# Optimization experiments

Hardware: AMD Instinct MI355X
Metric: run time of the kernel (lower is better)

## Reference

```python
import jax, jax.numpy as jnp
import numpy as np

B, S, D, H = 2048, 200, 64, 4
H1, H2 = 64, 32
F = 4 * D


def _prelu(x, a):
    return jnp.where(x > 0, x, a * x)


def setup_inputs() -> dict:
    key = jax.random.key(0)
    ks = jax.random.split(key, 12)
    inp = {
        "query": jax.random.normal(ks[0], (B, D), dtype=jnp.float32),
        "keys": jax.random.normal(ks[1], (B, S, D), dtype=jnp.float32),
        "keys_mask": jax.random.randint(ks[2], (B, S), 0, 2, dtype=jnp.int32),
        # per-head MLP params (torch Linear equivalent, stored as [in,out])
        "W1": jax.random.normal(ks[3], (H, F, H1), dtype=jnp.float32) / np.sqrt(F),
        "b1": jnp.zeros((H, H1), dtype=jnp.float32),
        "a1": jnp.full((H,), 0.25, dtype=jnp.float32),  # PReLU weight
        "W2": jax.random.normal(ks[4], (H, H1, H2), dtype=jnp.float32) / np.sqrt(H1),
        "b2": jnp.zeros((H, H2), dtype=jnp.float32),
        "a2": jnp.full((H,), 0.25, dtype=jnp.float32),
        "W3": jax.random.normal(ks[5], (H, H2), dtype=jnp.float32) / np.sqrt(H2),
        "b3": jnp.zeros((H,), dtype=jnp.float32),
        # output projection
        "Wo": jax.random.normal(ks[6], (D, D), dtype=jnp.float32) / np.sqrt(D),
        "bo": jnp.zeros((D,), dtype=jnp.float32),
    }
    return inp


def reference(query, keys, keys_mask, W1, b1, a1, W2, b2, a2, W3, b3, Wo, bo):
    # rich attention features: [keys, q, keys*q, keys-q] -> [B,S,4D]
    q = jnp.broadcast_to(query[:, None, :], keys.shape)
    x = jnp.concatenate([keys, q, keys * q, keys - q], axis=-1)
    # all heads at once: tiny per-head MLP with PReLU
    h = jnp.einsum('bsf,hfk->bhsk', x, W1) + b1[None, :, None, :]   # [B,H,S,H1]
    h = _prelu(h, a1[None, :, None, None])
    h = jnp.einsum('bhsk,hkm->bhsm', h, W2) + b2[None, :, None, :]  # [B,H,S,H2]
    h = _prelu(h, a2[None, :, None, None])
    scores = jnp.einsum('bhsm,hm->bhs', h, W3) + b3[None, :, None]  # [B,H,S]
    # mask + softmax + NaN->0 (all-masked rows)
    valid = (keys_mask != 0)[:, None, :]
    scores = jnp.where(valid, scores, -jnp.inf)
    w = jax.nn.softmax(scores, axis=-1)
    w = jnp.where(jnp.isnan(w), jnp.zeros_like(w), w)
    # weighted sum over keys, mean over heads
    out_h = jnp.einsum('bhs,bsd->bhd', w, keys)  # [B,H,D]
    combined = out_h.mean(axis=1)                # [B,D]
    return combined @ Wo + bo
```

## Files before the change

kernel.cpp:

```cpp
#include <hip/hip_runtime.h>
#include <math.h>

constexpr int B  = 2048;
constexpr int S  = 200;
constexpr int D  = 64;
constexpr int H  = 4;
constexpr int H1 = 64;
constexpr int H2 = 32;
constexpr int F  = 256;

constexpr int PK = 72;

typedef short bf16x8 __attribute__((ext_vector_type(8)));
typedef float f32x4  __attribute__((ext_vector_type(4)));
typedef unsigned uint4v __attribute__((ext_vector_type(4)));

__device__ __forceinline__ unsigned cvtpk(float a, float b) {
    unsigned r;
    asm volatile("v_cvt_pk_bf16_f32 %0, %1, %2" : "=v"(r) : "v"(a), "v"(b));
    return r;
}
__device__ __forceinline__ float lo16f(unsigned w) { return __builtin_bit_cast(float, w << 16); }
__device__ __forceinline__ float hi16f(unsigned w) { return __builtin_bit_cast(float, w & 0xffff0000u); }

constexpr size_t SAD_OFF = 0;
constexpr size_t SC_OFF  = SAD_OFF + 4 * 4096 * 4;
constexpr size_t SBD_OFF = SC_OFF  + 4 * 4096 * 4;
constexpr size_t W2I_OFF = SBD_OFF + 4 * 4096 * 4;

__global__ __launch_bounds__(256) void build_kernel(
    const float* __restrict__ W1, const float* __restrict__ W2,
    float* __restrict__ sad, float* __restrict__ sc, float* __restrict__ sbd,
    ushort* __restrict__ w2i)
{
    const int h    = blockIdx.x >> 1;
    const int half = blockIdx.x & 1;
    const int t = threadIdx.x;
    const float* w1h = W1 + (size_t)h * F * H1;

    {
        const int sl = half * 256 + t;
        const int f  = sl >> 6, l = sl & 63;
        const int mt = f & 3, kk = f >> 2;
        const int k  = 16 * mt + (l & 15);
        const int d0 = 32 * kk + ((l >> 4) << 3);
        float vs[8], vc[8], vb[8];
        #pragma unroll
        for (int j = 0; j < 8; ++j) {
            const int d = d0 + j;
            float A  = w1h[d * 64 + k];
            float Bv = w1h[(64 + d) * 64 + k];
            float C  = w1h[(128 + d) * 64 + k];
            float Dv = w1h[(192 + d) * 64 + k];
            vs[j] = A + Dv; vc[j] = C; vb[j] = Bv - Dv;
        }
        const size_t off = ((size_t)h * 512 + sl) * 8;
        *(f32x4*)&sad[off]     = *(f32x4*)&vs[0];
        *(f32x4*)&sad[off + 4] = *(f32x4*)&vs[4];
        *(f32x4*)&sc [off]     = *(f32x4*)&vc[0];
        *(f32x4*)&sc [off + 4] = *(f32x4*)&vc[4];
        *(f32x4*)&sbd[off]     = *(f32x4*)&vb[0];
        *(f32x4*)&sbd[off + 4] = *(f32x4*)&vb[4];
    }

    if (half == 0) {
        const int f2 = t >> 6, l = t & 63;
        const int mt2 = f2 & 1, w = f2 >> 1;
        const int m = 16 * mt2 + (l & 15), k20 = 32 * w + ((l >> 4) << 3);
        const float* w2h = W2 + (size_t)h * H1 * H2;
        uint4v u = { cvtpk(w2h[(k20 + 0) * 32 + m], w2h[(k20 + 1) * 32 + m]),
                     cvtpk(w2h[(k20 + 2) * 32 + m], w2h[(k20 + 3) * 32 + m]),
                     cvtpk(w2h[(k20 + 4) * 32 + m], w2h[(k20 + 5) * 32 + m]),
                     cvtpk(w2h[(k20 + 6) * 32 + m], w2h[(k20 + 7) * 32 + m]) };
        *(uint4v*)&w2i[((size_t)h * 4 + f2) * 512 + l * 8] = u;
    }
}

__global__ __launch_bounds__(256, 3) void fused_b_kernel(
    const float* __restrict__ query, const float* __restrict__ keys,
    const int* __restrict__ mask,
    const float* __restrict__ sad, const float* __restrict__ sc,
    const float* __restrict__ sbd, const ushort* __restrict__ w2i,
    const float* __restrict__ b1, const float* __restrict__ a1,
    const float* __restrict__ b2, const float* __restrict__ a2,
    const float* __restrict__ W3, const float* __restrict__ b3,
    const float* __restrict__ Wo, const float* __restrict__ bo,
    float* __restrict__ out)
{
    __shared__ ushort sK[200 * PK];
    __shared__ ushort relay[4][16 * PK];

    const int b    = blockIdx.x;
    const int t    = threadIdx.x;
    const int lane = t & 63;
    const int h    = t >> 6;
    const int g    = lane >> 4;
    const int ln16 = lane & 15;

    unsigned mbits = 0;
    {
        int mval[4];
        #pragma unroll
        for (int c = 0; c < 4; ++c) {
            int s = lane + 64 * c;
            mval[c] = (s < S) ? mask[(size_t)b * S + s] : 0;
        }
        #pragma unroll
        for (int st = 0; st < 13; ++st) {
            const int src = 16 * (st & 3) + ln16;
            int v = (st >> 2) == 0 ? __shfl(mval[0], src)
                  : (st >> 2) == 1 ? __shfl(mval[1], src)
                  : (st >> 2) == 2 ? __shfl(mval[2], src)
                  :                  __shfl(mval[3], src);
            mbits |= (v != 0) ? (1u << st) : 0u;
        }
    }

    {
        const float4* k4 = (const float4*)(keys + (size_t)b * S * D);
        float4 kv[6];
        #pragma unroll
        for (int i = 0; i < 6; ++i) kv[i] = k4[t + 256 * i];
        #pragma unroll
        for (int i = 0; i < 6; ++i) {
            const int idx = t + 256 * i;
            const int s = idx >> 4, dc = (idx & 15) * 4;
            *(uint2*)&sK[s * PK + dc] =
                make_uint2(cvtpk(kv[i].x, kv[i].y), cvtpk(kv[i].z, kv[i].w));
        }
        #pragma unroll
        for (int i = 0; i < 6; ++i) kv[i] = k4[t + 256 * (6 + i)];
        #pragma unroll
        for (int i = 0; i < 6; ++i) {
            const int idx = t + 256 * (6 + i);
            const int s = idx >> 4, dc = (idx & 15) * 4;
            *(uint2*)&sK[s * PK + dc] =
                make_uint2(cvtpk(kv[i].x, kv[i].y), cvtpk(kv[i].z, kv[i].w));
        }
        if (t < 128) {
            float4 kt = k4[3072 + t];
            const int idx = 3072 + t;
            const int s = idx >> 4, dc = (idx & 15) * 4;
            *(uint2*)&sK[s * PK + dc] =
                make_uint2(cvtpk(kt.x, kt.y), cvtpk(kt.z, kt.w));
        }
    }

    const float* qb = query + (size_t)b * D;
    bf16x8 wh[4][2];
    float qtp0 = 0.f, qtp1 = 0.f, qtp2 = 0.f, qtp3 = 0.f;
    #pragma unroll
    for (int kk = 0; kk < 2; ++kk) {
        const int d0 = 32 * kk + 8 * g;
        f32x4 q0 = *(const f32x4*)&qb[d0];
        f32x4 q1 = *(const f32x4*)&qb[d0 + 4];
        #pragma unroll
        for (int mt = 0; mt < 4; ++mt) {
            const int f = kk * 4 + mt;
            const size_t off = ((size_t)h * 512 + f * 64 + lane) * 8;
            f32x4 s0 = *(const f32x4*)&sad[off], s1 = *(const f32x4*)&sad[off + 4];
            f32x4 c0 = *(const f32x4*)&sc [off], c1 = *(const f32x4*)&sc [off + 4];
            f32x4 bd0 = *(const f32x4*)&sbd[off], bd1 = *(const f32x4*)&sbd[off + 4];
            float w0 = s0[0] + q0[0] * c0[0], w1 = s0[1] + q0[1] * c0[1];
            float w2 = s0[2] + q0[2] * c0[2], w3 = s0[3] + q0[3] * c0[3];
            float w4 = s1[0] + q1[0] * c1[0], w5 = s1[1] + q1[1] * c1[1];
            float w6 = s1[2] + q1[2] * c1[2], w7 = s1[3] + q1[3] * c1[3];
            uint4v u = { cvtpk(w0, w1), cvtpk(w2, w3), cvtpk(w4, w5), cvtpk(w6, w7) };
            wh[mt][kk] = __builtin_bit_cast(bf16x8, u);
            float d = q0[0]*bd0[0] + q0[1]*bd0[1] + q0[2]*bd0[2] + q0[3]*bd0[3]
                    + q1[0]*bd1[0] + q1[1]*bd1[1] + q1[2]*bd1[2] + q1[3]*bd1[3];
            if (mt == 0) qtp0 += d; else if (mt == 1) qtp1 += d;
            else if (mt == 2) qtp2 += d; else qtp3 += d;
        }
    }
    qtp0 += __shfl_xor(qtp0, 16); qtp0 += __shfl_xor(qtp0, 32);
    qtp1 += __shfl_xor(qtp1, 16); qtp1 += __shfl_xor(qtp1, 32);
    qtp2 += __shfl_xor(qtp2, 16); qtp2 += __shfl_xor(qtp2, 32);
    qtp3 += __shfl_xor(qtp3, 16); qtp3 += __shfl_xor(qtp3, 32);
    f32x4 qtv[4];
    #pragma unroll
    for (int mt = 0; mt < 4; ++mt) {
        float src = (mt == 0) ? qtp0 : (mt == 1) ? qtp1 : (mt == 2) ? qtp2 : qtp3;
        f32x4 b1v = *(const f32x4*)&b1[h * 64 + mt * 16 + 4 * g];
        f32x4 v;
        #pragma unroll
        for (int i = 0; i < 4; ++i) v[i] = __shfl(src, 4 * g + i) + b1v[i];
        qtv[mt] = v;
    }

    bf16x8 w2f[2][2];
    #pragma unroll
    for (int w = 0; w < 2; ++w)
        #pragma unroll
        for (int mt2 = 0; mt2 < 2; ++mt2)
            w2f[w][mt2] = *(const bf16x8*)&w2i[((size_t)h * 4 + w * 2 + mt2) * 512 + lane * 8];
    f32x4 b2v[2], w3v[2];
    #pragma unroll
    for (int mt2 = 0; mt2 < 2; ++mt2) {
        b2v[mt2] = *(const f32x4*)&b2[h * 32 + mt2 * 16 + 4 * g];
        w3v[mt2] = *(const f32x4*)&W3[h * 32 + mt2 * 16 + 4 * g];
    }
    const float a1v = a1[h], a2v = a2[h], b3v = b3[h];

    __syncthreads();

    ushort* myR = relay[h];
    float sc13[13];

    #pragma unroll
    for (int st = 0; st < 13; ++st) {
        int srow = st * 16 + ln16;
        srow = srow > 199 ? 199 : srow;
        bf16x8 bk0 = *(const bf16x8*)&sK[srow * PK + 0  + 8 * g];
        bf16x8 bk1 = *(const bf16x8*)&sK[srow * PK + 32 + 8 * g];

        f32x4 acc[4] = { qtv[0], qtv[1], qtv[2], qtv[3] };
        #pragma unroll
        for (int mt = 0; mt < 4; ++mt)
            acc[mt] = __builtin_amdgcn_mfma_f32_16x16x32_bf16(wh[mt][0], bk0, acc[mt], 0, 0, 0);
        #pragma unroll
        for (int mt = 0; mt < 4; ++mt)
            acc[mt] = __builtin_amdgcn_mfma_f32_16x16x32_bf16(wh[mt][1], bk1, acc[mt], 0, 0, 0);

        #pragma unroll
        for (int mt = 0; mt < 4; ++mt) {
            float v0 = fmaxf(acc[mt][0], acc[mt][0] * a1v);
            float v1 = fmaxf(acc[mt][1], acc[mt][1] * a1v);
            float v2 = fmaxf(acc[mt][2], acc[mt][2] * a1v);
            float v3 = fmaxf(acc[mt][3], acc[mt][3] * a1v);
            *(uint2*)&myR[ln16 * PK + mt * 16 + 4 * g] =
                make_uint2(cvtpk(v0, v1), cvtpk(v2, v3));
        }

        f32x4 acc2[2] = { b2v[0], b2v[1] };
        #pragma unroll
        for (int w = 0; w < 2; ++w) {
            bf16x8 Bh = *(const bf16x8*)&myR[ln16 * PK + w * 32 + 8 * g];
            #pragma unroll
            for (int mt2 = 0; mt2 < 2; ++mt2)
                acc2[mt2] = __builtin_amdgcn_mfma_f32_16x16x32_bf16(w2f[w][mt2], Bh, acc2[mt2], 0, 0, 0);
        }

        float part = 0.f;
        #pragma unroll
        for (int mt2 = 0; mt2 < 2; ++mt2) {
            #pragma unroll
            for (int i2 = 0; i2 < 4; ++i2) {
                float v = fmaxf(acc2[mt2][i2], acc2[mt2][i2] * a2v);
                part += v * w3v[mt2][i2];
            }
        }
        part += __shfl_xor(part, 16);
        part += __shfl_xor(part, 32);
        sc13[st] = part + b3v;
    }

    float* ws = (float*)myR;
    {
        float M = -INFINITY;
        #pragma unroll
        for (int st = 0; st < 13; ++st)
            if ((mbits >> st) & 1) M = fmaxf(M, sc13[st]);
        #pragma unroll
        for (int off = 1; off < 16; off <<= 1) M = fmaxf(M, __shfl_xor(M, off));
        float Z = 0.f;
        #pragma unroll
        for (int st = 0; st < 13; ++st)
            Z += ((mbits >> st) & 1) ? __expf(sc13[st] - M) : 0.f;
        #pragma unroll
        for (int off = 1; off < 16; off <<= 1) Z += __shfl_xor(Z, off);
        const float inv = Z > 0.f ? 1.f / Z : 0.f;
        if (g == 0) {
            #pragma unroll
            for (int st = 0; st < 13; ++st) {
                const int s = st * 16 + ln16;
                if (st < 12 || ln16 < 8)
                    ws[s] = ((mbits >> st) & 1) ? __expf(sc13[st] - M) * inv : 0.f;
            }
        }
    }

    {
        const int sg = lane >> 4, dq = ln16;
        float ax = 0.f, ay = 0.f, az = 0.f, aw = 0.f;
        #pragma unroll 5
        for (int i = 0; i < 50; ++i) {
            const int s = sg * 50 + i;
            const float w = ws[s];
            uint2 kv = *(const uint2*)&sK[s * PK + 4 * dq];
            ax += w * lo16f(kv.x); ay += w * hi16f(kv.x);
            az += w * lo16f(kv.y); aw += w * hi16f(kv.y);
        }
        ax += __shfl_xor(ax, 16); ay += __shfl_xor(ay, 16);
        az += __shfl_xor(az, 16); aw += __shfl_xor(aw, 16);
        ax += __shfl_xor(ax, 32); ay += __shfl_xor(ay, 32);
        az += __shfl_xor(az, 32); aw += __shfl_xor(aw, 32);
        if (lane < 16) {
            float4 o = { ax, ay, az, aw };
            *(float4*)&ws[200 + 4 * dq] = o;
        }
    }
    __syncthreads();

    {
        float p = 0.f;
        #pragma unroll
        for (int j = 0; j < 16; ++j) {
            const int d = 16 * h + j;
            const float cmb = 0.25f * (((const float*)relay[0])[200 + d]
                                     + ((const float*)relay[1])[200 + d]
                                     + ((const float*)relay[2])[200 + d]
                                     + ((const float*)relay[3])[200 + d]);
            p += cmb * Wo[d * 64 + lane];
        }
        ws[264 + lane] = p;
    }
    __syncthreads();
    if (t < 64) {
        float o = bo[t] + ((const float*)relay[0])[264 + t]
                        + ((const float*)relay[1])[264 + t]
                        + ((const float*)relay[2])[264 + t]
                        + ((const float*)relay[3])[264 + t];
        out[(size_t)b * D + t] = o;
    }
}

extern "C" void kernel_launch(void* const* d_in, const int* in_sizes, int n_in,
                              void* d_out, int out_size, void* d_ws, size_t ws_size,
                              hipStream_t stream) {
    const float* query = (const float*)d_in[0];
    const float* keys  = (const float*)d_in[1];
    const int*   mask  = (const int*)d_in[2];
    const float* W1 = (const float*)d_in[3];
    const float* b1 = (const float*)d_in[4];
    const float* a1 = (const float*)d_in[5];
    const float* W2 = (const float*)d_in[6];
    const float* b2 = (const float*)d_in[7];
    const float* a2 = (const float*)d_in[8];
    const float* W3 = (const float*)d_in[9];
    const float* b3 = (const float*)d_in[10];
    const float* Wo = (const float*)d_in[11];
    const float* bo = (const float*)d_in[12];

    float* out  = (float*)d_out;
    char*  ws   = (char*)d_ws;
    float* sad  = (float*)(ws + SAD_OFF);
    float* sc   = (float*)(ws + SC_OFF);
    float* sbd  = (float*)(ws + SBD_OFF);
    ushort* w2i = (ushort*)(ws + W2I_OFF);

    build_kernel<<<dim3(H * 2), 256, 0, stream>>>(W1, W2, sad, sc, sbd, w2i);
    fused_b_kernel<<<dim3(B), 256, 0, stream>>>(
        query, keys, mask, sad, sc, sbd, w2i, b1, a1, b2, a2, W3, b3,
        Wo, bo, out);
}
```

Baseline: 62.08 us.

## Permute W2 rows to enable 128-bit relay stores; read fp32 keys for weighted sum

```diff
diff --git a/kernel.cpp b/kernel.cpp
--- a/kernel.cpp
+++ b/kernel.cpp
@@ -20,8 +20,6 @@
     asm volatile("v_cvt_pk_bf16_f32 %0, %1, %2" : "=v"(r) : "v"(a), "v"(b));
     return r;
 }
-__device__ __forceinline__ float lo16f(unsigned w) { return __builtin_bit_cast(float, w << 16); }
-__device__ __forceinline__ float hi16f(unsigned w) { return __builtin_bit_cast(float, w & 0xffff0000u); }
 
 constexpr size_t SAD_OFF = 0;
 constexpr size_t SC_OFF  = SAD_OFF + 4 * 4096 * 4;
@@ -66,13 +64,19 @@
     if (half == 0) {
         const int f2 = t >> 6, l = t & 63;
         const int mt2 = f2 & 1, w = f2 >> 1;
-        const int m = 16 * mt2 + (l & 15), k20 = 32 * w + ((l >> 4) << 3);
+        const int m = 16 * mt2 + (l & 15);
+        const int c0 = 32 * w + ((l >> 4) << 3);
         const float* w2h = W2 + (size_t)h * H1 * H2;
-        uint4v u = { cvtpk(w2h[(k20 + 0) * 32 + m], w2h[(k20 + 1) * 32 + m]),
-                     cvtpk(w2h[(k20 + 2) * 32 + m], w2h[(k20 + 3) * 32 + m]),
-                     cvtpk(w2h[(k20 + 4) * 32 + m], w2h[(k20 + 5) * 32 + m]),
-                     cvtpk(w2h[(k20 + 6) * 32 + m], w2h[(k20 + 7) * 32 + m]) };
-        *(uint4v*)&w2i[((size_t)h * 4 + f2) * 512 + l * 8] = u;
+        unsigned u[4];
+        #pragma unroll
+        for (int j = 0; j < 4; ++j) {
+            const int ca = c0 + 2 * j, cb = ca + 1;
+            const int ka = 16 * (ca & 3) + (ca >> 2);
+            const int kb = 16 * (cb & 3) + (cb >> 2);
+            u[j] = cvtpk(w2h[ka * 32 + m], w2h[kb * 32 + m]);
+        }
+        uint4v v = { u[0], u[1], u[2], u[3] };
+        *(uint4v*)&w2i[((size_t)h * 4 + f2) * 512 + l * 8] = v;
     }
 }
 
@@ -222,14 +226,21 @@
         for (int mt = 0; mt < 4; ++mt)
             acc[mt] = __builtin_amdgcn_mfma_f32_16x16x32_bf16(wh[mt][1], bk1, acc[mt], 0, 0, 0);
 
-        #pragma unroll
-        for (int mt = 0; mt < 4; ++mt) {
-            float v0 = fmaxf(acc[mt][0], acc[mt][0] * a1v);
-            float v1 = fmaxf(acc[mt][1], acc[mt][1] * a1v);
-            float v2 = fmaxf(acc[mt][2], acc[mt][2] * a1v);
-            float v3 = fmaxf(acc[mt][3], acc[mt][3] * a1v);
-            *(uint2*)&myR[ln16 * PK + mt * 16 + 4 * g] =
-                make_uint2(cvtpk(v0, v1), cvtpk(v2, v3));
+        unsigned pk[8];
+        #pragma unroll
+        for (int i = 0; i < 4; ++i) {
+            float v0 = fmaxf(acc[0][i], acc[0][i] * a1v);
+            float v1 = fmaxf(acc[1][i], acc[1][i] * a1v);
+            float v2 = fmaxf(acc[2][i], acc[2][i] * a1v);
+            float v3 = fmaxf(acc[3][i], acc[3][i] * a1v);
+            pk[2*i]     = cvtpk(v0, v1);
+            pk[2*i + 1] = cvtpk(v2, v3);
+        }
+        {
+            uint4v wv0 = { pk[0], pk[1], pk[2], pk[3] };
+            uint4v wv1 = { pk[4], pk[5], pk[6], pk[7] };
+            *(uint4v*)&myR[ln16 * PK + 16 * g]     = wv0;
+            *(uint4v*)&myR[ln16 * PK + 16 * g + 8] = wv1;
         }
 
         f32x4 acc2[2] = { b2v[0], b2v[1] };
@@ -281,15 +292,16 @@
     }
 
     {
+        const float* kb = keys + (size_t)b * S * D;
         const int sg = lane >> 4, dq = ln16;
         float ax = 0.f, ay = 0.f, az = 0.f, aw = 0.f;
         #pragma unroll 5
         for (int i = 0; i < 50; ++i) {
             const int s = sg * 50 + i;
             const float w = ws[s];
-            uint2 kv = *(const uint2*)&sK[s * PK + 4 * dq];
-            ax += w * lo16f(kv.x); ay += w * hi16f(kv.x);
-            az += w * lo16f(kv.y); aw += w * hi16f(kv.y);
+            float4 kv = *(const float4*)&kb[s * 64 + 4 * dq];
+            ax += w * kv.x; ay += w * kv.y;
+            az += w * kv.z; aw += w * kv.w;
         }
         ax += __shfl_xor(ax, 16); ay += __shfl_xor(ay, 16);
         az += __shfl_xor(az, 16); aw += __shfl_xor(aw, 16);
```

New measurement: 70.16 us. +13.0%, slower.

## Keep layer-1 activations in registers as MFMA operands, drop LDS relay

Applied to the files above, without the earlier changes.

```diff
diff --git a/kernel.cpp b/kernel.cpp
--- a/kernel.cpp
+++ b/kernel.cpp
@@ -66,13 +66,17 @@
     if (half == 0) {
         const int f2 = t >> 6, l = t & 63;
         const int mt2 = f2 & 1, w = f2 >> 1;
-        const int m = 16 * mt2 + (l & 15), k20 = 32 * w + ((l >> 4) << 3);
+        const int m  = 16 * mt2 + (l & 15);
+        const int gg = l >> 4;
         const float* w2h = W2 + (size_t)h * H1 * H2;
-        uint4v u = { cvtpk(w2h[(k20 + 0) * 32 + m], w2h[(k20 + 1) * 32 + m]),
-                     cvtpk(w2h[(k20 + 2) * 32 + m], w2h[(k20 + 3) * 32 + m]),
-                     cvtpk(w2h[(k20 + 4) * 32 + m], w2h[(k20 + 5) * 32 + m]),
-                     cvtpk(w2h[(k20 + 6) * 32 + m], w2h[(k20 + 7) * 32 + m]) };
-        *(uint4v*)&w2i[((size_t)h * 4 + f2) * 512 + l * 8] = u;
+        const int ka = 32 * w + 4 * gg;
+        const int kb = ka + 16;
+        unsigned u0 = cvtpk(w2h[(ka + 0) * 32 + m], w2h[(ka + 1) * 32 + m]);
+        unsigned u1 = cvtpk(w2h[(ka + 2) * 32 + m], w2h[(ka + 3) * 32 + m]);
+        unsigned u2 = cvtpk(w2h[(kb + 0) * 32 + m], w2h[(kb + 1) * 32 + m]);
+        unsigned u3 = cvtpk(w2h[(kb + 2) * 32 + m], w2h[(kb + 3) * 32 + m]);
+        uint4v v = { u0, u1, u2, u3 };
+        *(uint4v*)&w2i[((size_t)h * 4 + f2) * 512 + l * 8] = v;
     }
 }
 
@@ -88,7 +92,7 @@
     float* __restrict__ out)
 {
     __shared__ ushort sK[200 * PK];
-    __shared__ ushort relay[4][16 * PK];
+    __shared__ float  exch[4][200];
 
     const int b    = blockIdx.x;
     const int t    = threadIdx.x;
@@ -204,7 +208,6 @@
 
     __syncthreads();
 
-    ushort* myR = relay[h];
     float sc13[13];
 
     #pragma unroll
@@ -222,24 +225,26 @@
         for (int mt = 0; mt < 4; ++mt)
             acc[mt] = __builtin_amdgcn_mfma_f32_16x16x32_bf16(wh[mt][1], bk1, acc[mt], 0, 0, 0);
 
+        unsigned P[4][2];
         #pragma unroll
         for (int mt = 0; mt < 4; ++mt) {
             float v0 = fmaxf(acc[mt][0], acc[mt][0] * a1v);
             float v1 = fmaxf(acc[mt][1], acc[mt][1] * a1v);
             float v2 = fmaxf(acc[mt][2], acc[mt][2] * a1v);
             float v3 = fmaxf(acc[mt][3], acc[mt][3] * a1v);
-            *(uint2*)&myR[ln16 * PK + mt * 16 + 4 * g] =
-                make_uint2(cvtpk(v0, v1), cvtpk(v2, v3));
-        }
+            P[mt][0] = cvtpk(v0, v1);
+            P[mt][1] = cvtpk(v2, v3);
+        }
+        uint4v bu0 = { P[0][0], P[0][1], P[1][0], P[1][1] };
+        uint4v bu1 = { P[2][0], P[2][1], P[3][0], P[3][1] };
+        bf16x8 Bh0 = __builtin_bit_cast(bf16x8, bu0);
+        bf16x8 Bh1 = __builtin_bit_cast(bf16x8, bu1);
 
         f32x4 acc2[2] = { b2v[0], b2v[1] };
-        #pragma unroll
-        for (int w = 0; w < 2; ++w) {
-            bf16x8 Bh = *(const bf16x8*)&myR[ln16 * PK + w * 32 + 8 * g];
-            #pragma unroll
-            for (int mt2 = 0; mt2 < 2; ++mt2)
-                acc2[mt2] = __builtin_amdgcn_mfma_f32_16x16x32_bf16(w2f[w][mt2], Bh, acc2[mt2], 0, 0, 0);
-        }
+        acc2[0] = __builtin_amdgcn_mfma_f32_16x16x32_bf16(w2f[0][0], Bh0, acc2[0], 0, 0, 0);
+        acc2[1] = __builtin_amdgcn_mfma_f32_16x16x32_bf16(w2f[0][1], Bh0, acc2[1], 0, 0, 0);
+        acc2[0] = __builtin_amdgcn_mfma_f32_16x16x32_bf16(w2f[1][0], Bh1, acc2[0], 0, 0, 0);
+        acc2[1] = __builtin_amdgcn_mfma_f32_16x16x32_bf16(w2f[1][1], Bh1, acc2[1], 0, 0, 0);
 
         float part = 0.f;
         #pragma unroll
@@ -255,7 +260,7 @@
         sc13[st] = part + b3v;
     }
 
-    float* ws = (float*)myR;
+    float* ws = exch[h];
     {
         float M = -INFINITY;
         #pragma unroll
@@ -297,7 +302,7 @@
         az += __shfl_xor(az, 32); aw += __shfl_xor(aw, 32);
         if (lane < 16) {
             float4 o = { ax, ay, az, aw };
-            *(float4*)&ws[200 + 4 * dq] = o;
+            *(float4*)&ws[4 * dq] = o;
         }
     }
     __syncthreads();
@@ -305,23 +310,22 @@
     {
         float p = 0.f;
         #pragma unroll
-        for (int j = 0; j < 16; ++j) {
-            const int d = 16 * h + j;
-            const float cmb = 0.25f * (((const float*)relay[0])[200 + d]
-                                     + ((const float*)relay[1])[200 + d]
-                                     + ((const float*)relay[2])[200 + d]
-                                     + ((const float*)relay[3])[200 + d]);
-            p += cmb * Wo[d * 64 + lane];
-        }
-        ws[264 + lane] = p;
-    }
-    __syncthreads();
-    if (t < 64) {
-        float o = bo[t] + ((const float*)relay[0])[264 + t]
-                        + ((const float*)relay[1])[264 + t]
-                        + ((const float*)relay[2])[264 + t]
-                        + ((const float*)relay[3])[264 + t];
-        out[(size_t)b * D + t] = o;
+        for (int jj = 0; jj < 4; ++jj) {
+            const int dp = 16 * g + 4 * jj;
+            f32x4 c0 = *(const f32x4*)&exch[0][dp];
+            f32x4 c1 = *(const f32x4*)&exch[1][dp];
+            f32x4 c2 = *(const f32x4*)&exch[2][dp];
+            f32x4 c3 = *(const f32x4*)&exch[3][dp];
+            #pragma unroll
+            for (int c = 0; c < 4; ++c) {
+                const float cmb = 0.25f * (c0[c] + c1[c] + c2[c] + c3[c]);
+                p += cmb * Wo[(dp + c) * 64 + 16 * h + ln16];
+            }
+        }
+        p += __shfl_xor(p, 16);
+        p += __shfl_xor(p, 32);
+        if (lane < 16)
+            out[(size_t)b * D + 16 * h + ln16] = p + bo[16 * h + ln16];
     }
 }
 
```

After: 60.08 us. -3.2%, faster.
